# Kernel tuning notes

Measured on AMD Instinct MI355X. Metric: run time of the kernel, lower is better.

## Reference

```python
import jax, jax.numpy as jnp
import numpy as np

B, NP, K, NC = 16, 4096, 20, 40  # graphs, points/graph, kNN k, classes
EPS = 1e-5


def knn_idx(x):
    # x: [B, Np, F] -> [B, Np, K] indices of K nearest neighbors (incl. self)
    sq = jnp.sum(x * x, axis=-1)                       # [B, Np]
    d = sq[:, :, None] + sq[:, None, :] - 2.0 * jnp.einsum('bnf,bmf->bnm', x, x)
    _, idx = jax.lax.top_k(-d, K)                      # smallest distances
    return idx


def gather_nbrs(x, idx):
    # x: [B, Np, F], idx: [B, Np, K] -> [B, Np, K, F]
    return jax.vmap(lambda xb, ib: xb[ib])(x, idx)


def bn_eval(h, g, b, m, v):
    return (h - m) * g * jax.lax.rsqrt(v + EPS) + b


def forward(pos, feat, W1, b1, g1, be1, m1, v1, W2, b2, g2, be2, m2, v2,
            W3, b3, Wc, bc, Wl, bl, Wa, ba, Wb, bb, Wo, bo):
    x0 = jnp.concatenate([pos, feat], axis=1).reshape(B, NP, 4)
    idx = knn_idx(x0)                                  # dynamic kNN in feature space

    # conv1: EdgeConv message h([x_i, x_j - x_i]) -> max over neighbors
    xj = gather_nbrs(x0, idx)                          # [B,Np,K,4]
    xi = jnp.broadcast_to(x0[:, :, None, :], xj.shape)
    e = jnp.concatenate([xi, xj - xi], axis=-1)        # [B,Np,K,8]
    h = jax.nn.relu(bn_eval(e @ W1 + b1, g1, be1, m1, v1))
    h = jax.nn.relu(bn_eval(h @ W2 + b2, g2, be2, m2, v2))
    h = h @ W3 + b3                                    # plain last layer
    x1 = jnp.max(h, axis=2)                            # [B,Np,64]

    # conv2: static EdgeConv on the same edge_index
    xj1 = gather_nbrs(x1, idx)                         # [B,Np,K,64]
    xi1 = jnp.broadcast_to(x1[:, :, None, :], xj1.shape)
    e2 = jnp.concatenate([xi1, xj1 - xi1], axis=-1)    # [B,Np,K,128]
    x2 = jnp.max(e2 @ Wc + bc, axis=2)                 # [B,Np,128]

    out1 = jnp.concatenate([x1, x2], axis=-1) @ Wl + bl  # [B,Np,1024]
    out2 = jnp.max(out1, axis=1)                       # global max pool -> [B,1024]

    h2 = jax.nn.relu(out2 @ Wa + ba)                   # dropout = identity (eval)
    h2 = jax.nn.relu(h2 @ Wb + bb)
    logits = h2 @ Wo + bo                              # [B,NC]
    return jax.nn.log_softmax(logits, axis=1)


def setup_inputs() -> dict:
    key = jax.random.key(0)
    ks = jax.random.split(key, 16)
    w = lambda k, i, o: jax.random.normal(k, (i, o), jnp.float32) * (1.0 / np.sqrt(i))
    z = lambda n: jnp.zeros((n,), jnp.float32)
    o = lambda n: jnp.ones((n,), jnp.float32)
    return {
        'pos': jax.random.normal(ks[0], (B * NP, 3), jnp.float32),
        'feat': jax.random.normal(ks[1], (B * NP, 1), jnp.float32),
        'W1': w(ks[2], 8, 64), 'b1': z(64), 'g1': o(64), 'be1': z(64), 'm1': z(64), 'v1': o(64),
        'W2': w(ks[3], 64, 64), 'b2': z(64), 'g2': o(64), 'be2': z(64), 'm2': z(64), 'v2': o(64),
        'W3': w(ks[4], 64, 64), 'b3': z(64),
        'Wc': w(ks[5], 128, 128), 'bc': z(128),
        'Wl': w(ks[6], 192, 1024), 'bl': z(1024),
        'Wa': w(ks[7], 1024, 512), 'ba': z(512),
        'Wb': w(ks[8], 512, 256), 'bb': z(256),
        'Wo': w(ks[9], 256, NC), 'bo': z(NC),
        'batch': jnp.repeat(jnp.arange(B), NP),
        'num_graphs': B,
    }


def reference(pos, feat, W1, b1, g1, be1, m1, v1, W2, b2, g2, be2, m2, v2,
              W3, b3, Wc, bc, Wl, bl, Wa, ba, Wb, bb, Wo, bo, batch, num_graphs):
    return forward(pos, feat, W1, b1, g1, be1, m1, v1, W2, b2, g2, be2, m2, v2,
                   W3, b3, Wc, bc, Wl, bl, Wa, ba, Wb, bb, Wo, bo)
```

## Files before the change

### kernel.cpp

```cpp
#include <hip/hip_runtime.h>
#include <math.h>

#define BGRAPH 16
#define NPG    4096
#define NPTS   (BGRAPH*NPG)
#define KNN    20
#define NC     40
#define EPSBN  1e-5f
#define SEG    8
#define SEGN   512
#define CPTS   4
#define BIGF   3.0e38f

typedef _Float16 half8 __attribute__((ext_vector_type(8)));
typedef _Float16 h4 __attribute__((ext_vector_type(4)));
typedef unsigned short ushort8 __attribute__((ext_vector_type(8)));
typedef float f32x4 __attribute__((ext_vector_type(4)));
typedef unsigned long long u64;

#define O_X0   0u
#define O_IDX  1048576u
#define O_X1   6291456u
#define O_WT   90177536u

__device__ __forceinline__ unsigned encf(float v) {
    unsigned u = __float_as_uint(v);
    return (u & 0x80000000u) ? ~u : (u | 0x80000000u);
}
__device__ __forceinline__ float decf(unsigned k) {
    unsigned u = (k & 0x80000000u) ? (k ^ 0x80000000u) : ~k;
    return __uint_as_float(u);
}
__device__ __forceinline__ unsigned ordf(float f) {
    unsigned u = __float_as_uint(f);
    return u ^ (((unsigned)((int)u >> 31)) | 0x80000000u);
}
__device__ __forceinline__ float distE(float4 xi, float4 xj, float sqh) {
    float e = sqh;
    e = fmaf(-xi.x, xj.x, e);
    e = fmaf(-xi.y, xj.y, e);
    e = fmaf(-xi.z, xj.z, e);
    e = fmaf(-xi.w, xj.w, e);
    return e;
}
__device__ __forceinline__ unsigned uminu(unsigned a, unsigned b) { return a < b ? a : b; }
__device__ __forceinline__ unsigned umed3(unsigned a, unsigned b, unsigned c) {
    unsigned d;
    asm("v_med3_u32 %0, %1, %2, %3" : "=v"(d) : "v"(a), "v"(b), "v"(c));
    return d;
}
__device__ __forceinline__ float fmed3(float a, float b, float c) {
    float d;
    asm("v_med3_f32 %0, %1, %2, %3" : "=v"(d) : "v"(a), "v"(b), "v"(c));
    return d;
}
__device__ __forceinline__ half8 hmax8(half8 a, half8 b) {
#if __has_builtin(__builtin_elementwise_max)
    return __builtin_elementwise_max(a, b);
#else
    half8 r;
    #pragma unroll
    for (int i = 0; i < 8; ++i) r[i] = a[i] > b[i] ? a[i] : b[i];
    return r;
#endif
}

#define TK_DECL unsigned w0=0xFFFFFFFFu,w1=0xFFFFFFFFu,w2=0xFFFFFFFFu,w3=0xFFFFFFFFu,w4=0xFFFFFFFFu, \
    w5=0xFFFFFFFFu,w6=0xFFFFFFFFu,w7=0xFFFFFFFFu,w8=0xFFFFFFFFu,w9=0xFFFFFFFFu, \
    w10=0xFFFFFFFFu,w11=0xFFFFFFFFu,w12=0xFFFFFFFFu,w13=0xFFFFFFFFu,w14=0xFFFFFFFFu, \
    w15=0xFFFFFFFFu,w16=0xFFFFFFFFu,w17=0xFFFFFFFFu,w18=0xFFFFFFFFu,w19=0xFFFFFFFFu;
#define TK_INSERT(uv_) { unsigned cu = (uv_); \
    w0  = umed3(w1,  w0,  cu); \
    w1  = umed3(w2,  w1,  cu); \
    w2  = umed3(w3,  w2,  cu); \
    w3  = umed3(w4,  w3,  cu); \
    w4  = umed3(w5,  w4,  cu); \
    w5  = umed3(w6,  w5,  cu); \
    w6  = umed3(w7,  w6,  cu); \
    w7  = umed3(w8,  w7,  cu); \
    w8  = umed3(w9,  w8,  cu); \
    w9  = umed3(w10, w9,  cu); \
    w10 = umed3(w11, w10, cu); \
    w11 = umed3(w12, w11, cu); \
    w12 = umed3(w13, w12, cu); \
    w13 = umed3(w14, w13, cu); \
    w14 = umed3(w15, w14, cu); \
    w15 = umed3(w16, w15, cu); \
    w16 = umed3(w17, w16, cu); \
    w17 = umed3(w18, w17, cu); \
    w18 = umed3(w19, w18, cu); \
    w19 = uminu(w19, cu); }

#define TKF_DECL float f0=BIGF,f1=BIGF,f2=BIGF,f3=BIGF,f4=BIGF,f5=BIGF,f6=BIGF,f7=BIGF,f8=BIGF,f9=BIGF, \
    f10=BIGF,f11=BIGF,f12=BIGF,f13=BIGF,f14=BIGF,f15=BIGF,f16=BIGF,f17=BIGF,f18=BIGF,f19=BIGF;
#define TKF_INSERT(dv_) { float cf = (dv_); \
    f0  = fmed3(f1,  f0,  cf); \
    f1  = fmed3(f2,  f1,  cf); \
    f2  = fmed3(f3,  f2,  cf); \
    f3  = fmed3(f4,  f3,  cf); \
    f4  = fmed3(f5,  f4,  cf); \
    f5  = fmed3(f6,  f5,  cf); \
    f6  = fmed3(f7,  f6,  cf); \
    f7  = fmed3(f8,  f7,  cf); \
    f8  = fmed3(f9,  f8,  cf); \
    f9  = fmed3(f10, f9,  cf); \
    f10 = fmed3(f11, f10, cf); \
    f11 = fmed3(f12, f11, cf); \
    f12 = fmed3(f13, f12, cf); \
    f13 = fmed3(f14, f13, cf); \
    f14 = fmed3(f15, f14, cf); \
    f15 = fmed3(f16, f15, cf); \
    f16 = fmed3(f17, f16, cf); \
    f17 = fmed3(f18, f17, cf); \
    f18 = fmed3(f19, f18, cf); \
    f19 = fminf(f19, cf); }

__global__ __launch_bounds__(256) void k_prep(
        const float* __restrict__ pos, const float* __restrict__ feat,
        const float* __restrict__ Wl,
        const float* __restrict__ W1, const float* __restrict__ b1,
        const float* __restrict__ g1, const float* __restrict__ be1,
        const float* __restrict__ m1, const float* __restrict__ v1,
        const float* __restrict__ W2, const float* __restrict__ b2,
        const float* __restrict__ g2, const float* __restrict__ be2,
        const float* __restrict__ m2, const float* __restrict__ v2,
        const float* __restrict__ W3, const float* __restrict__ Wc,
        float* __restrict__ x0, _Float16* __restrict__ Wlh,
        float* __restrict__ W1f, float* __restrict__ b1f,
        float* __restrict__ b2f,
        _Float16* __restrict__ W2t, _Float16* __restrict__ W3t,
        _Float16* __restrict__ Wuvh, unsigned* __restrict__ out2enc)
{
    __shared__ float tile[32][33];
    int bx = blockIdx.x, t = threadIdx.x;
    if (bx < 256) {
        int i = bx*256 + t;
        float4 v;
        v.x = pos[i*3+0]; v.y = pos[i*3+1]; v.z = pos[i*3+2]; v.w = feat[i];
        ((float4*)x0)[i] = v;
    } else if (bx < 256 + 192) {
        int w = bx - 256;
        int jb = (w & 31) * 32, kb = (w >> 5) * 32;
        int tx = t & 31, ty = t >> 5;
        #pragma unroll
        for (int r = 0; r < 32; r += 8)
            tile[ty + r][tx] = Wl[(size_t)(kb + ty + r)*1024 + jb + tx];
        __syncthreads();
        #pragma unroll
        for (int r = 0; r < 32; r += 8)
            Wlh[(size_t)(jb + ty + r)*192 + kb + tx] = (_Float16)tile[tx][ty + r];
    } else if (bx == 448) {
        for (int i = t; i < 64; i += 256) {
            float s1 = g1[i] * rsqrtf(v1[i] + EPSBN);
            b1f[i] = (b1[i] - m1[i]) * s1 + be1[i];
            float s2 = g2[i] * rsqrtf(v2[i] + EPSBN);
            b2f[i] = (b2[i] - m2[i]) * s2 + be2[i];
        }
        for (int i = t; i < 8*64; i += 256) {
            int c = i & 63;
            W1f[i] = W1[i] * (g1[c] * rsqrtf(v1[c] + EPSBN));
        }
        for (int i = t; i < 256*64; i += 256) {
            int c = i >> 6, d = i & 63;
            float v = (c < 128) ? (Wc[d*128 + c] - Wc[(64+d)*128 + c])
                                : Wc[(64+d)*128 + (c - 128)];
            Wuvh[i] = (_Float16)v;
        }
        for (int i = t; i < 16*1024; i += 256) out2enc[i] = 0u;
    } else {
        for (int i = t; i < 4096; i += 256) {
            int n = i & 63, k = i >> 6;
            float s2 = g2[n] * rsqrtf(v2[n] + EPSBN);
            W2t[(size_t)n*64 + k] = (_Float16)(W2[(size_t)k*64 + n] * s2);
            W3t[(size_t)n*64 + k] = (_Float16)W3[(size_t)k*64 + n];
        }
    }
}

__global__ __launch_bounds__(256, 2) void k_knn_part(const float* __restrict__ x0,
        unsigned* __restrict__ pkHi, unsigned* __restrict__ pkLo)
{
    __shared__ float4 pts[SEGN];
    __shared__ float  sqh[SEGN];
    int x  = blockIdx.x;
    int b  = x >> 7;
    int rb = (x >> 3) & 15;
    int s  = x & 7;
    int t  = threadIdx.x;
    int r  = b*NPG + rb*256 + t;
    float4 xi = ((const float4*)x0)[r];
    #pragma unroll
    for (int l = 0; l < SEGN/256; ++l) {
        float4 v = ((const float4*)x0)[b*NPG + s*SEGN + l*256 + t];
        pts[l*256 + t] = v;
        sqh[l*256 + t] = 0.5f*(v.x*v.x + v.y*v.y + v.z*v.z + v.w*v.w);
    }
    __syncthreads();

    TKF_DECL
    #pragma unroll 8
    for (int j = 0; j < SEGN; ++j) {
        float e = distE(xi, pts[j], sqh[j]);
        TKF_INSERT(e)
    }
    float tau = f0;

    int jbase = b*NPG + s*SEGN;
    unsigned* hcol = pkHi + (size_t)s*KNN*NPTS + r;
    unsigned* lcol = pkLo + (size_t)s*KNN*NPTS + r;
    unsigned cnt = 0, ecnt = 0;
    int e0 = 0, e1 = 0;
    #pragma unroll 4
    for (int j = 0; j < SEGN; ++j) {
        float e = distE(xi, pts[j], sqh[j]);
        if (e < tau) {
            hcol[(size_t)cnt*NPTS] = ordf(e);
            lcol[(size_t)cnt*NPTS] = (unsigned)(jbase + j);
            cnt++;
        } else if (e == tau) {
            if (ecnt == 0) e0 = j; else if (ecnt == 1) e1 = j;
            ecnt++;
        }
    }
    unsigned tauU = ordf(tau);
    if (cnt < KNN && ecnt > 0) { hcol[(size_t)cnt*NPTS] = tauU; lcol[(size_t)cnt*NPTS] = (unsigned)(jbase + e0); cnt++; }
    if (cnt < KNN && ecnt > 1) { hcol[(size_t)cnt*NPTS] = tauU; lcol[(size_t)cnt*NPTS] = (unsigned)(jbase + e1); cnt++; }
    while (cnt < KNN) {
        hcol[(size_t)cnt*NPTS] = 0xFFFFFFFFu;
        lcol[(size_t)cnt*NPTS] = (unsigned)r;
        cnt++;
    }
}

__global__ __launch_bounds__(256, 2) void k_knn_merge(const unsigned* __restrict__ pkHi,
        const unsigned* __restrict__ pkLo, int* __restrict__ idx)
{
    int r = blockIdx.x*256 + threadIdx.x;

    TK_DECL
    #pragma unroll 4
    for (int q = 0; q < SEG*KNN; ++q) {
        unsigned u = pkHi[(size_t)q*NPTS + r];
        TK_INSERT(u)
    }
    unsigned tauU = w0;

    unsigned cnt = 0, ecnt = 0;
    int e0 = 0, e1 = 0;
    int* o = idx + (size_t)r*KNN;
    #pragma unroll 4
    for (int q = 0; q < SEG*KNN; ++q) {
        unsigned u = pkHi[(size_t)q*NPTS + r];
        if (u < tauU) {
            if (cnt < KNN) o[cnt] = (int)pkLo[(size_t)q*NPTS + r];
            cnt++;
        } else if (u == tauU) {
            if (ecnt == 0) e0 = (int)pkLo[(size_t)q*NPTS + r];
            else if (ecnt == 1) e1 = (int)pkLo[(size_t)q*NPTS + r];
            ecnt++;
        }
    }
    if (cnt < KNN && ecnt > 0) { o[cnt] = e0; cnt++; }
    if (cnt < KNN && ecnt > 1) { o[cnt] = e1; cnt++; }
    while (cnt < KNN) { o[cnt] = r; cnt++; }
}

__global__ __launch_bounds__(256) void k_conv1(const float* __restrict__ x0,
        const int* __restrict__ idx,
        const float* __restrict__ W1f, const float* __restrict__ b1f,
        const _Float16* __restrict__ W2t, const float* __restrict__ b2f,
        const _Float16* __restrict__ W3t, const float* __restrict__ b3,
        _Float16* __restrict__ x1h)
{
    __shared__ _Float16 hsbuf[2*80*72];
    _Float16* hs0 = hsbuf;
    _Float16* hs1 = hsbuf + 80*72;
    int t = threadIdx.x;
    int w = t >> 6, l = t & 63;
    int lr = l & 15, lg = l >> 4;

    half8 w2f[2], w3f[2];
    #pragma unroll
    for (int ks = 0; ks < 2; ++ks) {
        w2f[ks] = *(const half8*)&W2t[(size_t)(w*16 + lr)*64 + ks*32 + lg*8];
        w3f[ks] = *(const half8*)&W3t[(size_t)(w*16 + lr)*64 + ks*32 + lg*8];
    }
    float b2s = b2f[w*16 + lr];
    float b3s = b3[w*16 + lr];

    {
        int c = l;
        float w1c[8];
        #pragma unroll
        for (int f = 0; f < 8; ++f) w1c[f] = W1f[f*64 + c];
        float b1c = b1f[c];
        int i = blockIdx.x*CPTS + w;
        float4 xi = ((const float4*)x0)[i];
        #pragma unroll 4
        for (int k = 0; k < KNN; ++k) {
            int j = idx[i*KNN + k];
            float4 xj = ((const float4*)x0)[j];
            float h = b1c + xi.x*w1c[0] + xi.y*w1c[1] + xi.z*w1c[2] + xi.w*w1c[3]
                          + (xj.x-xi.x)*w1c[4] + (xj.y-xi.y)*w1c[5]
                          + (xj.z-xi.z)*w1c[6] + (xj.w-xi.w)*w1c[7];
            hs0[(w*KNN + k)*72 + c] = (_Float16)fmaxf(h, 0.0f);
        }
    }
    __syncthreads();

    #pragma unroll
    for (int mt = 0; mt < 5; ++mt) {
        f32x4 acc = {b2s, b2s, b2s, b2s};
        #pragma unroll
        for (int ks = 0; ks < 2; ++ks) {
            half8 a = *(const half8*)&hs0[(mt*16 + lr)*72 + ks*32 + lg*8];
            acc = __builtin_amdgcn_mfma_f32_16x16x32_f16(a, w2f[ks], acc, 0, 0, 0);
        }
        #pragma unroll
        for (int jj = 0; jj < 4; ++jj)
            hs1[(mt*16 + lg*4 + jj)*72 + w*16 + lr] = (_Float16)fmaxf(acc[jj], 0.0f);
    }
    __syncthreads();

    float h3r[5][4];
    #pragma unroll
    for (int mt = 0; mt < 5; ++mt) {
        f32x4 acc = {b3s, b3s, b3s, b3s};
        #pragma unroll
        for (int ks = 0; ks < 2; ++ks) {
            half8 a = *(const half8*)&hs1[(mt*16 + lr)*72 + ks*32 + lg*8];
            acc = __builtin_amdgcn_mfma_f32_16x16x32_f16(a, w3f[ks], acc, 0, 0, 0);
        }
        #pragma unroll
        for (int jj = 0; jj < 4; ++jj) h3r[mt][jj] = acc[jj];
    }
    __syncthreads();

    float* h3f = (float*)hsbuf;
    #pragma unroll
    for (int mt = 0; mt < 5; ++mt) {
        #pragma unroll
        for (int jj = 0; jj < 4; ++jj)
            h3f[(mt*16 + lg*4 + jj)*66 + w*16 + lr] = h3r[mt][jj];
    }
    __syncthreads();

    {
        float m = -3.0e38f;
        #pragma unroll 4
        for (int k = 0; k < KNN; ++k)
            m = fmaxf(m, h3f[(w*KNN + k)*66 + l]);
        x1h[(size_t)(blockIdx.x*CPTS + w)*64 + l] = (_Float16)m;
    }
}

__global__ __launch_bounds__(256) void k_uv(const _Float16* __restrict__ x1h,
        const _Float16* __restrict__ Wuvh, const float* __restrict__ bc,
        _Float16* __restrict__ uvh)
{
    __shared__ _Float16 Ash[64][72];
    __shared__ _Float16 Bsh[256][72];
    int m0 = blockIdx.x * 64;
    int t  = threadIdx.x;
    {
        int row = t >> 2, q = t & 3;
        const ushort8* xp = (const ushort8*)(x1h + (size_t)(m0+row)*64 + q*16);
        *(ushort8*)&Ash[row][q*16]     = xp[0];
        *(ushort8*)&Ash[row][q*16 + 8] = xp[1];
    }
    {
        const ushort8* wp = (const ushort8*)(Wuvh + (size_t)t*64);
        #pragma unroll
        for (int ch = 0; ch < 8; ++ch)
            *(ushort8*)&Bsh[t][ch*8] = wp[ch];
    }
    __syncthreads();

    int w = t >> 6, l = t & 63;
    int lr = l & 15, lg = l >> 4;
    float bch[4];
    #pragma unroll
    for (int nt = 0; nt < 4; ++nt) {
        int col = w*64 + nt*16 + lr;
        bch[nt] = (col < 128) ? bc[col] : 0.0f;
    }
    #pragma unroll
    for (int mt = 0; mt < 4; ++mt) {
        #pragma unroll
        for (int nt = 0; nt < 4; ++nt) {
            f32x4 acc = {0.f, 0.f, 0.f, 0.f};
            #pragma unroll
            for (int ks = 0; ks < 2; ++ks) {
                half8 a = *(const half8*)&Ash[mt*16 + lr][ks*32 + lg*8];
                half8 b = *(const half8*)&Bsh[w*64 + nt*16 + lr][ks*32 + lg*8];
                acc = __builtin_amdgcn_mfma_f32_16x16x32_f16(a, b, acc, 0, 0, 0);
            }
            #pragma unroll
            for (int jj = 0; jj < 4; ++jj) {
                int row = m0 + mt*16 + lg*4 + jj;
                int col = w*64 + nt*16 + lr;
                uvh[(size_t)row*256 + col] = (_Float16)(acc[jj] + bch[nt]);
            }
        }
    }
}

__global__ __launch_bounds__(256) void k_out1(const _Float16* __restrict__ x1h,
        const _Float16* __restrict__ uvh, const int* __restrict__ idx,
        const _Float16* __restrict__ Wlh, const float* __restrict__ bl,
        unsigned* __restrict__ out2enc)
{
    __shared__ _Float16 Asd[64][208];
    __shared__ _Float16 Bsd[128][208];
    __shared__ float red[512];
    int m0 = blockIdx.x * 64;
    int t  = threadIdx.x;
    int g  = m0 >> 12;

    {
        int row = t >> 2, q = t & 3;
        const ushort8* xp = (const ushort8*)(x1h + (size_t)(m0+row)*64 + q*16);
        *(ushort8*)&Asd[row][q*16]     = xp[0];
        *(ushort8*)&Asd[row][q*16 + 8] = xp[1];
    }
    {
        int row = t >> 2, q = t & 3;
        const int* ip = idx + (size_t)(m0 + row)*KNN;
        const _Float16* vb = uvh + 128 + q*32;
        int j0 = ip[0];
        half8 vm0 = *(const half8*)(vb + (size_t)j0*256);
        half8 vm1 = *(const half8*)(vb + (size_t)j0*256 + 8);
        half8 vm2 = *(const half8*)(vb + (size_t)j0*256 + 16);
        half8 vm3 = *(const half8*)(vb + (size_t)j0*256 + 24);
        #pragma unroll 4
        for (int k = 1; k < KNN; ++k) {
            int j = ip[k];
            vm0 = hmax8(vm0, *(const half8*)(vb + (size_t)j*256));
            vm1 = hmax8(vm1, *(const half8*)(vb + (size_t)j*256 + 8));
            vm2 = hmax8(vm2, *(const half8*)(vb + (size_t)j*256 + 16));
            vm3 = hmax8(vm3, *(const half8*)(vb + (size_t)j*256 + 24));
        }
        const _Float16* ub = uvh + (size_t)(m0+row)*256 + q*32;
        half8 u0 = *(const half8*)(ub);
        half8 u1 = *(const half8*)(ub + 8);
        half8 u2 = *(const half8*)(ub + 16);
        half8 u3 = *(const half8*)(ub + 24);
        *(half8*)&Asd[row][64 + q*32]      = u0 + vm0;
        *(half8*)&Asd[row][64 + q*32 + 8]  = u1 + vm1;
        *(half8*)&Asd[row][64 + q*32 + 16] = u2 + vm2;
        *(half8*)&Asd[row][64 + q*32 + 24] = u3 + vm3;
    }

    int w  = t >> 6, l = t & 63;
    int lr = l & 15, lg = l >> 4;
    #pragma unroll 1
    for (int np = 0; np < 8; ++np) {
        int n0 = np * 128;
        __syncthreads();
        {
            int j = t >> 1, hf = t & 1;
            const ushort8* src = (const ushort8*)(Wlh + (size_t)(n0 + j)*192 + hf*96);
            #pragma unroll
            for (int ch = 0; ch < 12; ++ch)
                *(ushort8*)&Bsd[j][hf*96 + ch*8] = src[ch];
        }
        __syncthreads();

        f32x4 acc[8];
        #pragma unroll
        for (int f = 0; f < 8; ++f) acc[f] = (f32x4){0.f, 0.f, 0.f, 0.f};
        #pragma unroll 1
        for (int ks = 0; ks < 6; ++ks) {
            half8 a = *(const half8*)&Asd[w*16 + lr][ks*32 + lg*8];
            #pragma unroll
            for (int f = 0; f < 8; ++f) {
                half8 b = *(const half8*)&Bsd[f*16 + lr][ks*32 + lg*8];
                acc[f] = __builtin_amdgcn_mfma_f32_16x16x32_f16(a, b, acc[f], 0, 0, 0);
            }
        }
        float cmax[8];
        #pragma unroll
        for (int f = 0; f < 8; ++f) {
            float m = fmaxf(fmaxf(acc[f][0], acc[f][1]), fmaxf(acc[f][2], acc[f][3]));
            m = fmaxf(m, __shfl_xor(m, 16));
            m = fmaxf(m, __shfl_xor(m, 32));
            cmax[f] = m;
        }
        if (l < 16) {
            #pragma unroll
            for (int f = 0; f < 8; ++f) red[w*128 + f*16 + l] = cmax[f];
        }
        __syncthreads();
        if (t < 128) {
            float m = fmaxf(fmaxf(red[t], red[128 + t]), fmaxf(red[256 + t], red[384 + t]));
            m += bl[n0 + t];
            atomicMax(&out2enc[g*1024 + n0 + t], encf(m));
        }
    }
}

__global__ __launch_bounds__(256) void k_headA(const unsigned* __restrict__ out2enc,
        const float* __restrict__ Wa, const float* __restrict__ ba, float* __restrict__ s2g)
{
    __shared__ float s1[1024];
    __shared__ float part[8][32];
    int g = blockIdx.x >> 4, chunk = blockIdx.x & 15;
    int t = threadIdx.x;
    for (int i = t; i < 1024; i += 256) s1[i] = decf(out2enc[g*1024 + i]);
    __syncthreads();
    int col = chunk*32 + (t & 31);
    int seg = t >> 5;
    float a0 = 0.f, a1 = 0.f, a2 = 0.f, a3 = 0.f;
    int d0 = seg*128;
    #pragma unroll 8
    for (int d = 0; d < 128; d += 4) {
        a0 = fmaf(s1[d0+d+0], Wa[(size_t)(d0+d+0)*512 + col], a0);
        a1 = fmaf(s1[d0+d+1], Wa[(size_t)(d0+d+1)*512 + col], a1);
        a2 = fmaf(s1[d0+d+2], Wa[(size_t)(d0+d+2)*512 + col], a2);
        a3 = fmaf(s1[d0+d+3], Wa[(size_t)(d0+d+3)*512 + col], a3);
    }
    part[seg][t & 31] = (a0 + a1) + (a2 + a3);
    __syncthreads();
    if (t < 32) {
        float a = 0.f;
        #pragma unroll
        for (int s = 0; s < 8; ++s) a += part[s][t];
        s2g[g*512 + chunk*32 + t] = fmaxf(ba[chunk*32 + t] + a, 0.f);
    }
}

__global__ __launch_bounds__(256) void k_headB1(const float* __restrict__ s2g,
        const float* __restrict__ Wb, const float* __restrict__ bb, float* __restrict__ s3g)
{
    __shared__ float s2[512];
    __shared__ float part[4][64];
    int g = blockIdx.x >> 2, chunk = blockIdx.x & 3;
    int t = threadIdx.x;
    for (int i = t; i < 512; i += 256) s2[i] = s2g[g*512 + i];
    __syncthreads();
    int col = chunk*64 + (t & 63);
    int seg = t >> 6;
    float a0 = 0.f, a1 = 0.f, a2 = 0.f, a3 = 0.f;
    int d0 = seg*128;
    #pragma unroll 8
    for (int d = 0; d < 128; d += 4) {
        a0 = fmaf(s2[d0+d+0], Wb[(size_t)(d0+d+0)*256 + col], a0);
        a1 = fmaf(s2[d0+d+1], Wb[(size_t)(d0+d+1)*256 + col], a1);
        a2 = fmaf(s2[d0+d+2], Wb[(size_t)(d0+d+2)*256 + col], a2);
        a3 = fmaf(s2[d0+d+3], Wb[(size_t)(d0+d+3)*256 + col], a3);
    }
    part[seg][t & 63] = (a0 + a1) + (a2 + a3);
    __syncthreads();
    if (t < 64) {
        float a = part[0][t] + part[1][t] + part[2][t] + part[3][t];
        s3g[g*256 + chunk*64 + t] = fmaxf(bb[chunk*64 + t] + a, 0.f);
    }
}

__global__ __launch_bounds__(256) void k_headB2(const float* __restrict__ s3g,
        const float* __restrict__ Wo, const float* __restrict__ bo,
        float* __restrict__ out)
{
    __shared__ float s3[256];
    __shared__ float sl[NC];
    int g = blockIdx.x, t = threadIdx.x;
    s3[t] = s3g[g*256 + t];
    __syncthreads();
    if (t < NC) {
        float a = bo[t];
        #pragma unroll 8
        for (int d = 0; d < 256; ++d) a += s3[d] * Wo[d*NC + t];
        sl[t] = a;
    }
    __syncthreads();
    if (t < 64) {
        float v = (t < NC) ? sl[t] : -3.0e38f;
        float m = v;
        #pragma unroll
        for (int o2 = 32; o2 >= 1; o2 >>= 1) m = fmaxf(m, __shfl_xor(m, o2));
        float e = (t < NC) ? expf(sl[t] - m) : 0.f;
        float s = e;
        #pragma unroll
        for (int o2 = 32; o2 >= 1; o2 >>= 1) s += __shfl_xor(s, o2);
        float ls = logf(s) + m;
        if (t < NC) out[g*NC + t] = sl[t] - ls;
    }
}

extern "C" void kernel_launch(void* const* d_in, const int* in_sizes, int n_in,
                              void* d_out, int out_size, void* d_ws, size_t ws_size,
                              hipStream_t stream)
{
    const float* pos  = (const float*)d_in[0];
    const float* feat = (const float*)d_in[1];
    const float* W1 = (const float*)d_in[2];
    const float* b1 = (const float*)d_in[3];
    const float* g1 = (const float*)d_in[4];
    const float* be1= (const float*)d_in[5];
    const float* m1 = (const float*)d_in[6];
    const float* v1 = (const float*)d_in[7];
    const float* W2 = (const float*)d_in[8];
    const float* b2 = (const float*)d_in[9];
    const float* g2 = (const float*)d_in[10];
    const float* be2= (const float*)d_in[11];
    const float* m2 = (const float*)d_in[12];
    const float* v2 = (const float*)d_in[13];
    const float* W3 = (const float*)d_in[14];
    const float* b3 = (const float*)d_in[15];
    const float* Wc = (const float*)d_in[16];
    const float* bc = (const float*)d_in[17];
    const float* Wl = (const float*)d_in[18];
    const float* bl = (const float*)d_in[19];
    const float* Wa = (const float*)d_in[20];
    const float* ba = (const float*)d_in[21];
    const float* Wb = (const float*)d_in[22];
    const float* bb = (const float*)d_in[23];
    const float* Wo = (const float*)d_in[24];
    const float* bo = (const float*)d_in[25];
    float* out = (float*)d_out;

    char* ws = (char*)d_ws;
    float* x0  = (float*)(ws + O_X0);
    int*   idx = (int*)  (ws + O_IDX);
    _Float16* x1h = (_Float16*)(ws + O_X1);
    _Float16* uvh = (_Float16*)(ws + O_X1 + 8388608u);
    unsigned* pkHi = (unsigned*)(ws + O_X1);
    unsigned* pkLo = pkHi + (size_t)SEG*KNN*NPTS;
    float* W1f = (float*)(ws + O_WT);
    float* b1f = W1f + 512;
    float* W2f = b1f + 64;
    float* b2f = W2f + 4096;
    _Float16* Wuvh = (_Float16*)(b2f + 64);
    unsigned* out2enc = (unsigned*)((float*)(b2f + 64) + 64*256);
    _Float16* Wlh = (_Float16*)(ws + O_WT + 262144);
    float* s2g = (float*)(ws + O_WT + 262144 + 393216);
    _Float16* W2t = (_Float16*)(ws + O_WT + 262144 + 393216 + 32768);
    _Float16* W3t = W2t + 4096;
    float* s3g = (float*)(ws + O_WT + 262144 + 393216 + 49152);

    k_prep <<<450, 256, 0, stream>>>(pos, feat, Wl,
                                     W1,b1,g1,be1,m1,v1, W2,b2,g2,be2,m2,v2, W3, Wc,
                                     x0, Wlh, W1f,b1f,b2f, W2t,W3t, Wuvh,out2enc);
    k_knn_part <<<BGRAPH*16*SEG, 256, 0, stream>>>(x0, pkHi, pkLo);
    k_knn_merge<<<NPTS/256, 256, 0, stream>>>(pkHi, pkLo, idx);
    k_conv1<<<NPTS/CPTS, 256, 0, stream>>>(x0, idx, W1f, b1f, W2t, b2f, W3t, b3, x1h);
    k_uv   <<<NPTS/64, 256, 0, stream>>>(x1h, Wuvh, bc, uvh);
    k_out1 <<<1024, 256, 0, stream>>>(x1h, uvh, idx, Wlh, bl, out2enc);
    k_headA<<<BGRAPH*16, 256, 0, stream>>>(out2enc, Wa, ba, s2g);
    k_headB1<<<BGRAPH*4, 256, 0, stream>>>(s2g, Wb, bb, s3g);
    k_headB2<<<BGRAPH, 256, 0, stream>>>(s3g, Wo, bo, out);
}
```

Baseline: 663.5 us.

## Keep only top-12 per kNN segment with exact brute-force fallback in merge

Each of the 8 per-graph segments now keeps 12 candidates instead of 20, which shrinks the partial insertion network and the candidate buffers the merge kernel reads. The merge tracks each segment's largest kept value. If any segment could have held more true neighbors than it kept, it falls back to a full brute-force scan over the graph's 4096 points for that query. This makes the common case cheaper while staying exact, but any query that hits the fallback is slow and causes wave divergence.

```diff
diff --git a/kernel.cpp b/kernel.cpp
--- a/kernel.cpp
+++ b/kernel.cpp
@@ -9,6 +9,7 @@
 #define EPSBN  1e-5f
 #define SEG    8
 #define SEGN   512
+#define SEGK   12
 #define CPTS   4
 #define BIGF   3.0e38f
 
@@ -44,6 +45,7 @@
     return e;
 }
 __device__ __forceinline__ unsigned uminu(unsigned a, unsigned b) { return a < b ? a : b; }
+__device__ __forceinline__ unsigned umaxu(unsigned a, unsigned b) { return a < b ? b : a; }
 __device__ __forceinline__ unsigned umed3(unsigned a, unsigned b, unsigned c) {
     unsigned d;
     asm("v_med3_u32 %0, %1, %2, %3" : "=v"(d) : "v"(a), "v"(b), "v"(c));
@@ -115,6 +117,22 @@
     f18 = fmed3(f19, f18, cf); \
     f19 = fminf(f19, cf); }
 
+#define TKS_DECL float g0=BIGF,g1=BIGF,g2=BIGF,g3=BIGF,g4=BIGF,g5=BIGF, \
+    g6=BIGF,g7=BIGF,g8=BIGF,g9=BIGF,g10=BIGF,g11=BIGF;
+#define TKS_INSERT(dv_) { float cf = (dv_); \
+    g0  = fmed3(g1,  g0,  cf); \
+    g1  = fmed3(g2,  g1,  cf); \
+    g2  = fmed3(g3,  g2,  cf); \
+    g3  = fmed3(g4,  g3,  cf); \
+    g4  = fmed3(g5,  g4,  cf); \
+    g5  = fmed3(g6,  g5,  cf); \
+    g6  = fmed3(g7,  g6,  cf); \
+    g7  = fmed3(g8,  g7,  cf); \
+    g8  = fmed3(g9,  g8,  cf); \
+    g9  = fmed3(g10, g9,  cf); \
+    g10 = fmed3(g11, g10, cf); \
+    g11 = fminf(g11, cf); }
+
 __global__ __launch_bounds__(256) void k_prep(
         const float* __restrict__ pos, const float* __restrict__ feat,
         const float* __restrict__ Wl,
@@ -197,17 +215,17 @@
     }
     __syncthreads();
 
-    TKF_DECL
+    TKS_DECL
     #pragma unroll 8
     for (int j = 0; j < SEGN; ++j) {
         float e = distE(xi, pts[j], sqh[j]);
-        TKF_INSERT(e)
-    }
-    float tau = f0;
+        TKS_INSERT(e)
+    }
+    float tau = g0;
 
     int jbase = b*NPG + s*SEGN;
-    unsigned* hcol = pkHi + (size_t)s*KNN*NPTS + r;
-    unsigned* lcol = pkLo + (size_t)s*KNN*NPTS + r;
+    unsigned* hcol = pkHi + (size_t)s*SEGK*NPTS + r;
+    unsigned* lcol = pkLo + (size_t)s*SEGK*NPTS + r;
     unsigned cnt = 0, ecnt = 0;
     int e0 = 0, e1 = 0;
     #pragma unroll 4
@@ -223,46 +241,89 @@
         }
     }
     unsigned tauU = ordf(tau);
-    if (cnt < KNN && ecnt > 0) { hcol[(size_t)cnt*NPTS] = tauU; lcol[(size_t)cnt*NPTS] = (unsigned)(jbase + e0); cnt++; }
-    if (cnt < KNN && ecnt > 1) { hcol[(size_t)cnt*NPTS] = tauU; lcol[(size_t)cnt*NPTS] = (unsigned)(jbase + e1); cnt++; }
-    while (cnt < KNN) {
+    if (cnt < SEGK && ecnt > 0) { hcol[(size_t)cnt*NPTS] = tauU; lcol[(size_t)cnt*NPTS] = (unsigned)(jbase + e0); cnt++; }
+    if (cnt < SEGK && ecnt > 1) { hcol[(size_t)cnt*NPTS] = tauU; lcol[(size_t)cnt*NPTS] = (unsigned)(jbase + e1); cnt++; }
+    while (cnt < SEGK) {
         hcol[(size_t)cnt*NPTS] = 0xFFFFFFFFu;
         lcol[(size_t)cnt*NPTS] = (unsigned)r;
         cnt++;
     }
 }
 
-__global__ __launch_bounds__(256, 2) void k_knn_merge(const unsigned* __restrict__ pkHi,
-        const unsigned* __restrict__ pkLo, int* __restrict__ idx)
+#define SEG_LOAD(S, SM) { unsigned km = 0u; \
+    _Pragma("unroll") \
+    for (int k2 = 0; k2 < SEGK; ++k2) { \
+        unsigned u = pkHi[((size_t)((S)*SEGK + k2))*NPTS + r]; \
+        TK_INSERT(u) \
+        km = umaxu(km, u); \
+    } \
+    SM = km; }
+
+__global__ __launch_bounds__(256, 2) void k_knn_merge(const float* __restrict__ x0,
+        const unsigned* __restrict__ pkHi, const unsigned* __restrict__ pkLo,
+        int* __restrict__ idx)
 {
     int r = blockIdx.x*256 + threadIdx.x;
 
     TK_DECL
-    #pragma unroll 4
-    for (int q = 0; q < SEG*KNN; ++q) {
-        unsigned u = pkHi[(size_t)q*NPTS + r];
-        TK_INSERT(u)
-    }
+    unsigned sm0, sm1, sm2, sm3, sm4, sm5, sm6, sm7;
+    SEG_LOAD(0, sm0) SEG_LOAD(1, sm1) SEG_LOAD(2, sm2) SEG_LOAD(3, sm3)
+    SEG_LOAD(4, sm4) SEG_LOAD(5, sm5) SEG_LOAD(6, sm6) SEG_LOAD(7, sm7)
     unsigned tauU = w0;
 
-    unsigned cnt = 0, ecnt = 0;
-    int e0 = 0, e1 = 0;
+    bool flag = (sm0 <= tauU) || (sm1 <= tauU) || (sm2 <= tauU) || (sm3 <= tauU) ||
+                (sm4 <= tauU) || (sm5 <= tauU) || (sm6 <= tauU) || (sm7 <= tauU);
+
     int* o = idx + (size_t)r*KNN;
-    #pragma unroll 4
-    for (int q = 0; q < SEG*KNN; ++q) {
-        unsigned u = pkHi[(size_t)q*NPTS + r];
-        if (u < tauU) {
-            if (cnt < KNN) o[cnt] = (int)pkLo[(size_t)q*NPTS + r];
-            cnt++;
-        } else if (u == tauU) {
-            if (ecnt == 0) e0 = (int)pkLo[(size_t)q*NPTS + r];
-            else if (ecnt == 1) e1 = (int)pkLo[(size_t)q*NPTS + r];
-            ecnt++;
-        }
-    }
-    if (cnt < KNN && ecnt > 0) { o[cnt] = e0; cnt++; }
-    if (cnt < KNN && ecnt > 1) { o[cnt] = e1; cnt++; }
-    while (cnt < KNN) { o[cnt] = r; cnt++; }
+    if (!flag) {
+        unsigned cnt = 0, ecnt = 0;
+        int e0 = 0, e1 = 0;
+        #pragma unroll 4
+        for (int q = 0; q < SEG*SEGK; ++q) {
+            unsigned u = pkHi[(size_t)q*NPTS + r];
+            if (u < tauU) {
+                if (cnt < KNN) o[cnt] = (int)pkLo[(size_t)q*NPTS + r];
+                cnt++;
+            } else if (u == tauU) {
+                if (ecnt == 0) e0 = (int)pkLo[(size_t)q*NPTS + r];
+                else if (ecnt == 1) e1 = (int)pkLo[(size_t)q*NPTS + r];
+                ecnt++;
+            }
+        }
+        if (cnt < KNN && ecnt > 0) { o[cnt] = e0; cnt++; }
+        if (cnt < KNN && ecnt > 1) { o[cnt] = e1; cnt++; }
+        while (cnt < KNN) { o[cnt] = r; cnt++; }
+    } else {
+        int gb = r & ~(NPG - 1);
+        float4 xi = ((const float4*)x0)[r];
+        TKF_DECL
+        #pragma unroll 1
+        for (int j = 0; j < NPG; ++j) {
+            float4 xj = ((const float4*)x0)[gb + j];
+            float sh = 0.5f*(xj.x*xj.x + xj.y*xj.y + xj.z*xj.z + xj.w*xj.w);
+            float e = distE(xi, xj, sh);
+            TKF_INSERT(e)
+        }
+        float tauF = f0;
+        unsigned cnt = 0, ecnt = 0;
+        int a0 = 0, a1 = 0;
+        #pragma unroll 1
+        for (int j = 0; j < NPG; ++j) {
+            float4 xj = ((const float4*)x0)[gb + j];
+            float sh = 0.5f*(xj.x*xj.x + xj.y*xj.y + xj.z*xj.z + xj.w*xj.w);
+            float e = distE(xi, xj, sh);
+            if (e < tauF) {
+                if (cnt < KNN) o[cnt] = gb + j;
+                cnt++;
+            } else if (e == tauF) {
+                if (ecnt == 0) a0 = gb + j; else if (ecnt == 1) a1 = gb + j;
+                ecnt++;
+            }
+        }
+        if (cnt < KNN && ecnt > 0) { o[cnt] = a0; cnt++; }
+        if (cnt < KNN && ecnt > 1) { o[cnt] = a1; cnt++; }
+        while (cnt < KNN) { o[cnt] = r; cnt++; }
+    }
 }
 
 __global__ __launch_bounds__(256) void k_conv1(const float* __restrict__ x0,
@@ -625,7 +686,7 @@
     _Float16* x1h = (_Float16*)(ws + O_X1);
     _Float16* uvh = (_Float16*)(ws + O_X1 + 8388608u);
     unsigned* pkHi = (unsigned*)(ws + O_X1);
-    unsigned* pkLo = pkHi + (size_t)SEG*KNN*NPTS;
+    unsigned* pkLo = pkHi + (size_t)SEG*SEGK*NPTS;
     float* W1f = (float*)(ws + O_WT);
     float* b1f = W1f + 512;
     float* W2f = b1f + 64;
@@ -642,7 +703,7 @@
                                      W1,b1,g1,be1,m1,v1, W2,b2,g2,be2,m2,v2, W3, Wc,
                                      x0, Wlh, W1f,b1f,b2f, W2t,W3t, Wuvh,out2enc);
     k_knn_part <<<BGRAPH*16*SEG, 256, 0, stream>>>(x0, pkHi, pkLo);
-    k_knn_merge<<<NPTS/256, 256, 0, stream>>>(pkHi, pkLo, idx);
+    k_knn_merge<<<NPTS/256, 256, 0, stream>>>(x0, pkHi, pkLo, idx);
     k_conv1<<<NPTS/CPTS, 256, 0, stream>>>(x0, idx, W1f, b1f, W2t, b2f, W3t, b3, x1h);
     k_uv   <<<NPTS/64, 256, 0, stream>>>(x1h, Wuvh, bc, uvh);
     k_out1 <<<1024, 256, 0, stream>>>(x1h, uvh, idx, Wlh, bl, out2enc);
```

Measured after the change: 540.7 us, median of 2. -18.5%, faster.
